# Kernel tuning notes

Hardware: AMD Instinct MI355X
Metric: run time of the kernel (lower is better)

## Reference

```python
import jax, jax.numpy as jnp
import numpy as np

B, T, E, H, W = 2, 1024, 1024, 8, 31
D = 2 * W + 1  # head dim must equal 2*window_size+1 for the rel-pos broadcast


def _ln(x, w, b):
    mu = jnp.mean(x, axis=-1, keepdims=True)
    var = jnp.mean(jnp.square(x - mu), axis=-1, keepdims=True)
    return (x - mu) * jax.lax.rsqrt(var + 1e-5) * w + b


def setup_inputs() -> dict:
    key = jax.random.key(0)
    k = jax.random.split(key, 8)
    s = 0.02
    return {
        "x": jax.random.normal(k[0], (B, T, E // 2), jnp.float32),
        "ln1_w": jnp.ones(E, jnp.float32), "ln1_b": jnp.zeros(E, jnp.float32),
        "qkv_w": jax.random.normal(k[1], (3 * H * D, E), jnp.float32) * s,
        "qkv_b": jnp.zeros(3 * H * D, jnp.float32),
        "rel_pos": jax.random.normal(k[2], (D, D), jnp.float32) * s,
        "proj_w": jax.random.normal(k[3], (E, H * D), jnp.float32) * s,
        "proj_b": jnp.zeros(E, jnp.float32),
        "ln2_w": jnp.ones(E, jnp.float32), "ln2_b": jnp.zeros(E, jnp.float32),
        "fc_w": jax.random.normal(k[4], (4 * E, E), jnp.float32) * s,
        "fc_b": jnp.zeros(4 * E, jnp.float32),
        "cproj_w": jax.random.normal(k[5], (E, 4 * E), jnp.float32) * s,
        "cproj_b": jnp.zeros(E, jnp.float32),
    }


def reference(x, ln1_w, ln1_b, qkv_w, qkv_b, rel_pos, proj_w, proj_b,
              ln2_w, ln2_b, fc_w, fc_b, cproj_w, cproj_b):
    # --- RotaryEmbedding: angle = x * inv_freq; out = cat(sin, cos) -> [B,T,E]
    dim = 2 * x.shape[-1]
    inv_freq = 1.0 / 10000.0 ** (jnp.arange(0, dim, 2, dtype=jnp.float32) / dim)
    ang = x * inv_freq
    xr = jnp.concatenate([jnp.sin(ang), jnp.cos(ang)], axis=-1)  # [B,T,E]

    # --- custom windowed attention on ln_1(xr)
    h = _ln(xr, ln1_w, ln1_b)
    qkv = h @ qkv_w.T + qkv_b                       # [B,T,3*H*D]
    q, k, v = jnp.split(qkv, 3, axis=-1)

    def heads(t):
        return t.reshape(B, T, H, D).transpose(0, 2, 1, 3)  # [B,H,T,D]

    q, k, v = heads(q), heads(k), heads(v)
    # per-token q-outer-k scores (einsum '...bd,...bv->...bdv'): [B,H,T,D,D]
    scores = jnp.einsum('bhtd,bhtv->bhtdv', q, k)
    # rel-pos bias: Embedding lookup at offsets -W..W (negative indices wrap)
    bias = rel_pos[jnp.arange(-W, W + 1) % D]       # [D, D] == [2W+1, d_model]
    attn = jax.nn.softmax(scores + bias, axis=-2)   # softmax over non-canonical axis
    out = jnp.einsum('bhtdv,bhtv->bhtd', attn, v)   # apply per-token attn matrix to v
    out = out.transpose(0, 2, 1, 3).reshape(B, T, H * D)
    xa = xr + out @ proj_w.T + proj_b               # residual

    # --- MLP
    h2 = _ln(xa, ln2_w, ln2_b)
    m = jax.nn.gelu(h2 @ fc_w.T + fc_b, approximate=False) @ cproj_w.T + cproj_b
    return xa + m
```

## Files before the change

### kernel.cpp

```cpp
#include <hip/hip_runtime.h>
#include <hip/hip_bf16.h>


typedef __bf16 bf16;
typedef bf16 bf16x8 __attribute__((ext_vector_type(8)));
typedef bf16 bf16x4 __attribute__((ext_vector_type(4)));
typedef bf16 bf16x2 __attribute__((ext_vector_type(2)));
typedef float f32x4 __attribute__((ext_vector_type(4)));

__device__ __forceinline__ float rdlane(float x, int l)
{
    return __int_as_float(__builtin_amdgcn_readlane(__float_as_int(x), l));
}

__global__ __launch_bounds__(256) void rotary_ln_kernel(
    const float* __restrict__ x, const float* __restrict__ w,
    const float* __restrict__ b, float* __restrict__ xr, bf16* __restrict__ Y)
{
    const int row = blockIdx.x;
    const int tid = threadIdx.x;
    float2 xv = *(const float2*)(x + (size_t)row * 512 + tid * 2);
    float i0 = exp2f(-(float)(2*tid)     * 0.025952563241307518f);
    float i1 = exp2f(-(float)(2*tid + 1) * 0.025952563241307518f);
    float a0 = xv.x * i0, a1 = xv.y * i1;
    float s0 = sinf(a0), s1 = sinf(a1);
    float c0 = cosf(a0), c1 = cosf(a1);
    *(float2*)(xr + (size_t)row * 1024 + tid*2)       = make_float2(s0, s1);
    *(float2*)(xr + (size_t)row * 1024 + 512 + tid*2) = make_float2(c0, c1);
    float s  = s0 + s1 + c0 + c1;
    float ss = s0*s0 + s1*s1 + c0*c0 + c1*c1;
    #pragma unroll
    for (int off = 32; off > 0; off >>= 1) {
        s  += __shfl_down(s, off);
        ss += __shfl_down(ss, off);
    }
    __shared__ float rs[4], rss[4];
    int wave = tid >> 6, lane = tid & 63;
    if (lane == 0) { rs[wave] = s; rss[wave] = ss; }
    __syncthreads();
    s  = rs[0] + rs[1] + rs[2] + rs[3];
    ss = rss[0] + rss[1] + rss[2] + rss[3];
    float mu   = s * (1.f / 1024.f);
    float var  = ss * (1.f / 1024.f) - mu * mu;
    float rstd = rsqrtf(var + 1e-5f);
    float2 w0 = *(const float2*)(w + tid*2);
    float2 b0 = *(const float2*)(b + tid*2);
    float2 w1 = *(const float2*)(w + 512 + tid*2);
    float2 b1 = *(const float2*)(b + 512 + tid*2);
    bf16x2 y0, y1;
    y0[0] = (bf16)((s0 - mu) * rstd * w0.x + b0.x);
    y0[1] = (bf16)((s1 - mu) * rstd * w0.y + b0.y);
    y1[0] = (bf16)((c0 - mu) * rstd * w1.x + b1.x);
    y1[1] = (bf16)((c1 - mu) * rstd * w1.y + b1.y);
    *(bf16x2*)(Y + (size_t)row * 1024 + tid*2)       = y0;
    *(bf16x2*)(Y + (size_t)row * 1024 + 512 + tid*2) = y1;
}

__device__ __forceinline__ void conv_chunk(
    const float* __restrict__ src, bf16* __restrict__ dst,
    int ci, int N, int K, int Kp)
{
    int kpc = Kp >> 3;
    int r  = ci / kpc;
    int kc = (ci - r * kpc) << 3;
    bf16x8 o;
    if (r < N && kc < K) {
        float4 f0 = *(const float4*)(src + (size_t)r * K + kc);
        float4 f1 = *(const float4*)(src + (size_t)r * K + kc + 4);
        o[0]=(bf16)f0.x; o[1]=(bf16)f0.y; o[2]=(bf16)f0.z; o[3]=(bf16)f0.w;
        o[4]=(bf16)f1.x; o[5]=(bf16)f1.y; o[6]=(bf16)f1.z; o[7]=(bf16)f1.w;
    } else {
        #pragma unroll
        for (int j = 0; j < 8; ++j) o[j] = (bf16)0.f;
    }
    *(bf16x8*)(dst + (size_t)r * Kp + kc) = o;
}

__global__ __launch_bounds__(256) void conv_all_kernel(
    const float* __restrict__ qkv_w, const float* __restrict__ proj_w,
    const float* __restrict__ fc_w,  const float* __restrict__ cproj_w,
    const float* __restrict__ qkv_b,
    bf16* __restrict__ wqkv, bf16* __restrict__ wproj,
    bf16* __restrict__ wfc,  bf16* __restrict__ wcproj,
    float* __restrict__ qkvb_p)
{
    if (blockIdx.x == 5120) {
        for (int i = threadIdx.x; i < 1536; i += 256)
            qkvb_p[i] = (i < 1512) ? qkv_b[i] : 0.f;
        return;
    }
    int idx = blockIdx.x * 256 + threadIdx.x;
    if      (idx < 196608)  conv_chunk(qkv_w,   wqkv,   idx,          1512, 1024, 1024);
    else if (idx < 262144)  conv_chunk(proj_w,  wproj,  idx - 196608, 1024,  504,  512);
    else if (idx < 786432)  conv_chunk(fc_w,    wfc,    idx - 262144, 4096, 1024, 1024);
    else                    conv_chunk(cproj_w, wcproj, idx - 786432, 1024, 4096, 4096);
}

template<int N> __device__ __forceinline__ void vmwait()
{
    if constexpr      (N==0) asm volatile("s_waitcnt vmcnt(0)" ::: "memory");
    else if constexpr (N==3) asm volatile("s_waitcnt vmcnt(3)" ::: "memory");
    else if constexpr (N==4) asm volatile("s_waitcnt vmcnt(4)" ::: "memory");
}
__device__ __forceinline__ void lgkmwait0()
{
    asm volatile("s_waitcnt lgkmcnt(0)" ::: "memory");
}
__device__ __forceinline__ void hw_barrier()
{
    asm volatile("s_barrier" ::: "memory");
}
__device__ __forceinline__ void gload16(const char* src, char* ldsdst)
{
    __builtin_amdgcn_global_load_lds(
        (const __attribute__((address_space(1))) void*)src,
        (__attribute__((address_space(3))) void*)ldsdst, 16, 0, 0);
}
__device__ __forceinline__ float gelu_exact(float v)
{
    return 0.5f * v * (1.f + erff(v * 0.70710678118654752f));
}

template<int EPI>
__global__ __launch_bounds__(256, 3) void gemm9_kernel(
    const bf16* __restrict__ A, const bf16* __restrict__ Wt,
    const float* __restrict__ bias, bf16* __restrict__ Cb,
    int N, int Kp, int ksplit)
{
    __shared__ __align__(16) char lds[3][16384];

    const int tid  = threadIdx.x;
    const int w    = tid >> 6;
    const int lane = tid & 63;

    const int gx = gridDim.x, gy = gridDim.y;
    const int nwg = gx * gy * gridDim.z;
    const int chunk = nwg >> 3;
    int id = (blockIdx.z * gy + blockIdx.y) * gx + blockIdx.x;
    int sw = (id & 7) * chunk + (id >> 3);
    const int bx = sw % gx;
    const int t2 = sw / gx;
    const int by = t2 % gy;
    const int bz = t2 / gy;

    const int row0 = by * 128;
    const int col0 = bx * 128;
    const int wr = (w >> 1) * 64;
    const int wc = (w & 1) * 64;
    const int rl = lane & 15;
    const int slotR = lane >> 4;

    const size_t strideBy = (size_t)Kp * 2;
    const size_t kz = (size_t)bz * ksplit * 2;
    const char* Abase = (const char*)A  + (size_t)row0 * strideBy + kz;
    const char* Wbase = (const char*)Wt + (size_t)col0 * strideBy + kz;

    size_t srcA[2];
    #pragma unroll
    for (int i = 0; i < 2; ++i) {
        int ch = i * 256 + tid;
        int r  = ch >> 2;
        int s  = (ch & 3) ^ ((r >> 1) & 3);
        srcA[i] = (size_t)r * strideBy + (size_t)(s << 4);
    }

    f32x4 acc[4][4] = {};

    auto STAGE = [&](int buf, int kt) {
        const char* ab = Abase + (size_t)kt * 64;
        const char* wb = Wbase + (size_t)kt * 64;
        #pragma unroll
        for (int i = 0; i < 2; ++i)
            gload16(ab + srcA[i], &lds[buf][0]    + (i * 256 + tid) * 16);
        #pragma unroll
        for (int i = 0; i < 2; ++i)
            gload16(wb + srcA[i], &lds[buf][8192] + (i * 256 + tid) * 16);
    };

    const int niter = ksplit >> 5;
    STAGE(0, 0);
    STAGE(1, 1);
    vmwait<4>();
    hw_barrier();

    int cur = 0, stg = 2;
    for (int kt = 0; kt < niter; ++kt) {
        if (kt + 2 < niter) STAGE(stg, kt + 2);
        const char* base = lds[cur];
        bf16x8 af[4], bfr[4];
        #pragma unroll
        for (int mi = 0; mi < 4; ++mi) {
            int r = wr + mi * 16 + rl;
            af[mi] = *(const bf16x8*)
                (base + (r << 6) + ((slotR ^ ((r >> 1) & 3)) << 4));
        }
        #pragma unroll
        for (int nj = 0; nj < 4; ++nj) {
            int r = wc + nj * 16 + rl;
            bfr[nj] = *(const bf16x8*)
                (base + 8192 + (r << 6) + ((slotR ^ ((r >> 1) & 3)) << 4));
        }
        hw_barrier();
        lgkmwait0();
        __builtin_amdgcn_s_setprio(1);
        #pragma unroll
        for (int mi = 0; mi < 4; ++mi)
            #pragma unroll
            for (int nj = 0; nj < 4; ++nj)
                acc[mi][nj] = __builtin_amdgcn_mfma_f32_16x16x32_bf16(
                    af[mi], bfr[nj], acc[mi][nj], 0, 0, 0);
        __builtin_amdgcn_s_setprio(0);

        if (kt + 1 < niter) {
            if (kt + 2 < niter) vmwait<4>();
            else                vmwait<0>();
            hw_barrier();
        }
        cur = (cur == 2) ? 0 : cur + 1;
        stg = (stg == 2) ? 0 : stg + 1;
    }

    const int rq = (lane >> 4) * 4;
    bf16* Cbz = Cb;
    if (EPI == 3) Cbz += (size_t)bz * 2048 * N;
    #pragma unroll
    for (int mi = 0; mi < 4; ++mi) {
        #pragma unroll
        for (int rj = 0; rj < 4; ++rj) {
            int row = row0 + wr + mi*16 + rq + rj;
            #pragma unroll
            for (int nj = 0; nj < 4; ++nj) {
                int col = col0 + wc + nj*16 + rl;
                float c = acc[mi][nj][rj];
                size_t off = (size_t)row * N + col;
                if (EPI == 0)      Cbz[off] = (bf16)(c + bias[col]);
                else if (EPI == 1) Cbz[off] = (bf16)gelu_exact(c + bias[col]);
                else               Cbz[off] = (bf16)c;
            }
        }
    }
}

template<int EPI>
__global__ __launch_bounds__(256, 4) void gemm7_kernel(
    const bf16* __restrict__ A, const bf16* __restrict__ Wt,
    const float* __restrict__ bias, bf16* __restrict__ Cb,
    int N, int Kp, int ksplit)
{
    __shared__ __align__(16) char lds[3][12288];

    const int tid  = threadIdx.x;
    const int w    = tid >> 6;
    const int lane = tid & 63;

    const int gx = gridDim.x, gy = gridDim.y;
    const int nwg = gx * gy * gridDim.z;
    const int chunk = nwg >> 3;
    int id = (blockIdx.z * gy + blockIdx.y) * gx + blockIdx.x;
    int sw = (id & 7) * chunk + (id >> 3);
    const int bx = sw % gx;
    const int t2 = sw / gx;
    const int by = t2 % gy;
    const int bz = t2 / gy;

    const int row0 = by * 64;
    const int col0 = bx * 128;
    const int wr = (w >> 1) * 32;
    const int wc = (w & 1) * 64;
    const int rl = lane & 15;
    const int slotR = lane >> 4;

    const size_t strideBy = (size_t)Kp * 2;
    const size_t kz = (size_t)bz * ksplit * 2;
    const char* Abase = (const char*)A  + (size_t)row0 * strideBy + kz;
    const char* Wbase = (const char*)Wt + (size_t)col0 * strideBy + kz;

    const int arow = tid >> 2;
    const size_t srcA0 = (size_t)arow * strideBy
                       + (size_t)(((tid & 3) ^ ((arow >> 1) & 3)) << 4);
    size_t srcB[2];
    #pragma unroll
    for (int i = 0; i < 2; ++i) {
        int o = (i * 256 + tid) * 16;
        int r = o >> 6;
        int s = ((o & 63) >> 4) ^ ((r >> 1) & 3);
        srcB[i] = (size_t)r * strideBy + (size_t)(s << 4);
    }

    f32x4 acc[2][4] = {};

    auto STAGE = [&](int buf, int kt) {
        const char* ab = Abase + (size_t)kt * 64;
        const char* wb = Wbase + (size_t)kt * 64;
        gload16(ab + srcA0, &lds[buf][0] + tid * 16);
        #pragma unroll
        for (int i = 0; i < 2; ++i)
            gload16(wb + srcB[i], &lds[buf][4096] + (i * 256 + tid) * 16);
    };

    const int niter = ksplit >> 5;
    STAGE(0, 0);
    STAGE(1, 1);
    vmwait<3>();
    hw_barrier();

    int cur = 0, stg = 2;
    for (int kt = 0; kt < niter; ++kt) {
        if (kt + 2 < niter) STAGE(stg, kt + 2);
        const char* base = lds[cur];
        bf16x8 af[2], bfr[4];
        #pragma unroll
        for (int mi = 0; mi < 2; ++mi) {
            int r = wr + mi * 16 + rl;
            af[mi] = *(const bf16x8*)
                (base + (r << 6) + ((slotR ^ ((r >> 1) & 3)) << 4));
        }
        #pragma unroll
        for (int nj = 0; nj < 4; ++nj) {
            int r = wc + nj * 16 + rl;
            bfr[nj] = *(const bf16x8*)
                (base + 4096 + (r << 6) + ((slotR ^ ((r >> 1) & 3)) << 4));
        }
        __builtin_amdgcn_s_setprio(1);
        #pragma unroll
        for (int mi = 0; mi < 2; ++mi)
            #pragma unroll
            for (int nj = 0; nj < 4; ++nj)
                acc[mi][nj] = __builtin_amdgcn_mfma_f32_16x16x32_bf16(
                    af[mi], bfr[nj], acc[mi][nj], 0, 0, 0);
        __builtin_amdgcn_s_setprio(0);

        if (kt + 1 < niter) {
            lgkmwait0();
            if (kt + 2 < niter) vmwait<3>();
            else                vmwait<0>();
            hw_barrier();
        }
        cur = (cur == 2) ? 0 : cur + 1;
        stg = (stg == 2) ? 0 : stg + 1;
    }

    const int rq = (lane >> 4) * 4;
    bf16* Cbz = Cb;
    if (EPI == 3) Cbz += (size_t)bz * 2048 * N;
    #pragma unroll
    for (int mi = 0; mi < 2; ++mi) {
        #pragma unroll
        for (int rj = 0; rj < 4; ++rj) {
            int row = row0 + wr + mi*16 + rq + rj;
            #pragma unroll
            for (int nj = 0; nj < 4; ++nj) {
                int col = col0 + wc + nj*16 + rl;
                float c = acc[mi][nj][rj];
                size_t off = (size_t)row * N + col;
                if (EPI == 0)      Cbz[off] = (bf16)(c + bias[col]);
                else if (EPI == 1) Cbz[off] = (bf16)gelu_exact(c + bias[col]);
                else               Cbz[off] = (bf16)c;
            }
        }
    }
}

template<int P>
__global__ __launch_bounds__(256) void reduce_kernel(
    const bf16* __restrict__ parts, const float* __restrict__ bias,
    const float* R, float* out)
{
    int row = blockIdx.x;
    int c = threadIdx.x * 4;
    size_t off = (size_t)row * 1024 + c;
    float4 bv = *(const float4*)(bias + c);
    float4 o = *(const float4*)(R + off);
    o.x += bv.x; o.y += bv.y; o.z += bv.z; o.w += bv.w;
    #pragma unroll
    for (int p = 0; p < P; ++p) {
        bf16x4 v = *(const bf16x4*)(parts + (size_t)p * 2048 * 1024 + off);
        o.x += (float)v[0]; o.y += (float)v[1];
        o.z += (float)v[2]; o.w += (float)v[3];
    }
    *(float4*)(out + off) = o;
}

__global__ __launch_bounds__(256) void reduceln_kernel(
    const bf16* __restrict__ parts, const float* __restrict__ bias,
    const float* __restrict__ R, const float* __restrict__ lnw,
    const float* __restrict__ lnb, float* __restrict__ out,
    bf16* __restrict__ Y)
{
    int row = blockIdx.x;
    int c = threadIdx.x * 4;
    size_t off = (size_t)row * 1024 + c;
    float4 bv = *(const float4*)(bias + c);
    float4 o  = *(const float4*)(R + off);
    o.x += bv.x; o.y += bv.y; o.z += bv.z; o.w += bv.w;
    #pragma unroll
    for (int p = 0; p < 2; ++p) {
        bf16x4 v = *(const bf16x4*)(parts + (size_t)p * 2048 * 1024 + off);
        o.x += (float)v[0]; o.y += (float)v[1];
        o.z += (float)v[2]; o.w += (float)v[3];
    }
    *(float4*)(out + off) = o;
    float s  = o.x + o.y + o.z + o.w;
    float ss = o.x*o.x + o.y*o.y + o.z*o.z + o.w*o.w;
    #pragma unroll
    for (int of = 32; of > 0; of >>= 1) {
        s  += __shfl_down(s, of);
        ss += __shfl_down(ss, of);
    }
    __shared__ float rs[4], rss[4];
    int wave = threadIdx.x >> 6, lane = threadIdx.x & 63;
    if (lane == 0) { rs[wave] = s; rss[wave] = ss; }
    __syncthreads();
    s  = rs[0] + rs[1] + rs[2] + rs[3];
    ss = rss[0] + rss[1] + rss[2] + rss[3];
    float mu  = s * (1.f / 1024.f);
    float var = ss * (1.f / 1024.f) - mu * mu;
    float rstd = rsqrtf(var + 1e-5f);
    float4 wv = *(const float4*)(lnw + c);
    float4 lb = *(const float4*)(lnb + c);
    bf16 y[4];
    y[0] = (bf16)((o.x - mu) * rstd * wv.x + lb.x);
    y[1] = (bf16)((o.y - mu) * rstd * wv.y + lb.y);
    y[2] = (bf16)((o.z - mu) * rstd * wv.z + lb.z);
    y[3] = (bf16)((o.w - mu) * rstd * wv.w + lb.w);
    *(uint2*)(Y + (size_t)row * 1024 + c) = *(uint2*)y;
}

__global__ __launch_bounds__(1024) void attn3_kernel(
    const bf16* __restrict__ qkv, const float* __restrict__ rel_pos,
    bf16* __restrict__ outp)
{
    __shared__ float bR[4096];
    __shared__ float bT[4096];
    for (int i = threadIdx.x; i < 4096; i += 1024) {
        int d = i >> 6, v = i & 63;
        float val = (d < 63 && v < 63)
                  ? rel_pos[((d + 32) % 63) * 63 + v] * 1.4426950408889634f
                  : -1e30f;
        bR[(d << 6) + (((v >> 2) ^ (d & 15)) << 2) + (v & 3)] = val;
        bT[(v << 6) + (((d >> 2) ^ (v & 15)) << 2) + (d & 3)] = val;
    }
    __syncthreads();

    const int wave = threadIdx.x >> 6;
    const int lane = threadIdx.x & 63;
    const int tk  = blockIdx.x * 16 + wave;
    const int row = tk >> 3;
    const int h   = tk & 7;
    const bf16* base = qkv + (size_t)row * 1536 + h * 63;
    float q_own = 0.f, k_own = 0.f, v_own = 0.f;
    if (lane < 63) {
        q_own = (float)base[lane] * 1.4426950408889634f;
        k_own = (float)base[504 + lane];
        v_own = (float)base[1008 + lane];
    }

    const float* myT = bT + (lane << 6);
    const int sw = lane & 15;
    float z0 = 0.f, z1 = 0.f, z2 = 0.f, z3 = 0.f;
    #pragma unroll
    for (int g = 0; g < 16; ++g) {
        f32x4 bb = *(const f32x4*)(myT + ((g ^ sw) << 2));
        z0 += __builtin_amdgcn_exp2f(fmaf(rdlane(q_own, 4*g + 0), k_own, bb[0]));
        z1 += __builtin_amdgcn_exp2f(fmaf(rdlane(q_own, 4*g + 1), k_own, bb[1]));
        z2 += __builtin_amdgcn_exp2f(fmaf(rdlane(q_own, 4*g + 2), k_own, bb[2]));
        z3 += __builtin_amdgcn_exp2f(fmaf(rdlane(q_own, 4*g + 3), k_own, bb[3]));
    }
    float Z = (z0 + z1) + (z2 + z3);
    float w_own = (lane < 63) ? v_own / Z : 0.f;

    const float* myR = bR + (lane << 6);
    float a0 = 0.f, a1 = 0.f, a2 = 0.f, a3 = 0.f;
    #pragma unroll
    for (int g = 0; g < 16; ++g) {
        f32x4 bb = *(const f32x4*)(myR + ((g ^ sw) << 2));
        a0 = fmaf(__builtin_amdgcn_exp2f(fmaf(q_own, rdlane(k_own, 4*g + 0), bb[0])),
                  rdlane(w_own, 4*g + 0), a0);
        a1 = fmaf(__builtin_amdgcn_exp2f(fmaf(q_own, rdlane(k_own, 4*g + 1), bb[1])),
                  rdlane(w_own, 4*g + 1), a1);
        a2 = fmaf(__builtin_amdgcn_exp2f(fmaf(q_own, rdlane(k_own, 4*g + 2), bb[2])),
                  rdlane(w_own, 4*g + 2), a2);
        a3 = fmaf(__builtin_amdgcn_exp2f(fmaf(q_own, rdlane(k_own, 4*g + 3), bb[3])),
                  rdlane(w_own, 4*g + 3), a3);
    }
    float acc = (a0 + a1) + (a2 + a3);

    if (lane < 63)
        outp[(size_t)row * 512 + h*63 + lane] = (bf16)acc;
    if (h == 7 && lane == 63) {
        #pragma unroll
        for (int j = 0; j < 8; ++j)
            outp[(size_t)row * 512 + 504 + j] = (bf16)0.f;
    }
}

extern "C" void kernel_launch(void* const* d_in, const int* in_sizes, int n_in,
                              void* d_out, int out_size, void* d_ws, size_t ws_size,
                              hipStream_t stream)
{
    const float* x       = (const float*)d_in[0];
    const float* ln1_w   = (const float*)d_in[1];
    const float* ln1_b   = (const float*)d_in[2];
    const float* qkv_w   = (const float*)d_in[3];
    const float* qkv_b   = (const float*)d_in[4];
    const float* rel_pos = (const float*)d_in[5];
    const float* proj_w  = (const float*)d_in[6];
    const float* proj_b  = (const float*)d_in[7];
    const float* ln2_w   = (const float*)d_in[8];
    const float* ln2_b   = (const float*)d_in[9];
    const float* fc_w    = (const float*)d_in[10];
    const float* fc_b    = (const float*)d_in[11];
    const float* cproj_w = (const float*)d_in[12];
    const float* cproj_b = (const float*)d_in[13];
    float* out = (float*)d_out;

    char* p = (char*)d_ws;
    float* xr      = (float*)p;            p += (size_t)2048*1024*4;
    bf16*  h_bf    = (bf16*)p;             p += (size_t)2048*1024*2;
    bf16*  wqkv    = (bf16*)p;             p += (size_t)1536*1024*2;
    bf16*  wproj   = (bf16*)p;             p += (size_t)1024*512*2;
    bf16*  wfc     = (bf16*)p;             p += (size_t)4096*1024*2;
    bf16*  wcproj  = (bf16*)p;             p += (size_t)1024*4096*2;
    float* qkvb_p  = (float*)p;            p += 8192;
    bf16*  attn_bf = (bf16*)p;             p += (size_t)2048*512*2;
    bf16*  qkvb    = (bf16*)p;
    bf16*  fc_act  = (bf16*)p;
    bf16*  proj_part = qkvb;
    bf16*  cp_part = (bf16*)d_ws;

    conv_all_kernel<<<5121, 256, 0, stream>>>(qkv_w, proj_w, fc_w, cproj_w, qkv_b,
                                              wqkv, wproj, wfc, wcproj, qkvb_p);
    rotary_ln_kernel<<<2048, 256, 0, stream>>>(x, ln1_w, ln1_b, xr, h_bf);
    gemm7_kernel<0><<<dim3(12,32,1), 256, 0, stream>>>(h_bf, wqkv, qkvb_p,
                                                       qkvb, 1536, 1024, 1024);
    attn3_kernel<<<1024, 1024, 0, stream>>>(qkvb, rel_pos, attn_bf);
    gemm7_kernel<3><<<dim3(8,32,2), 256, 0, stream>>>(attn_bf, wproj, nullptr,
                                                      proj_part, 1024, 512, 256);
    reduceln_kernel<<<2048, 256, 0, stream>>>(proj_part, proj_b, xr,
                                              ln2_w, ln2_b, out, h_bf);
    gemm9_kernel<1><<<dim3(32,16,1), 256, 0, stream>>>(h_bf, wfc, fc_b,
                                                       fc_act, 4096, 1024, 1024);
    gemm9_kernel<3><<<dim3(8,16,4), 256, 0, stream>>>(fc_act, wcproj, nullptr,
                                                      cp_part, 1024, 4096, 1024);
    reduce_kernel<4><<<2048, 256, 0, stream>>>(cp_part, cproj_b, out, out);
}
```

Baseline: 136.9 us.

## Use 512-thread 8-wave blocks for MLP GEMMs and drop mid-loop barrier

```diff
diff --git a/kernel.cpp b/kernel.cpp
--- a/kernel.cpp
+++ b/kernel.cpp
@@ -99,6 +99,7 @@
 template<int N> __device__ __forceinline__ void vmwait()
 {
     if constexpr      (N==0) asm volatile("s_waitcnt vmcnt(0)" ::: "memory");
+    else if constexpr (N==2) asm volatile("s_waitcnt vmcnt(2)" ::: "memory");
     else if constexpr (N==3) asm volatile("s_waitcnt vmcnt(3)" ::: "memory");
     else if constexpr (N==4) asm volatile("s_waitcnt vmcnt(4)" ::: "memory");
 }
@@ -122,7 +123,7 @@
 }
 
 template<int EPI>
-__global__ __launch_bounds__(256, 3) void gemm9_kernel(
+__global__ __launch_bounds__(512, 4) void gemm11_kernel(
     const bf16* __restrict__ A, const bf16* __restrict__ Wt,
     const float* __restrict__ bias, bf16* __restrict__ Cb,
     int N, int Kp, int ksplit)
@@ -132,6 +133,10 @@
     const int tid  = threadIdx.x;
     const int w    = tid >> 6;
     const int lane = tid & 63;
+    const int wm   = w >> 2;
+    const int wn   = w & 3;
+    const int rl   = lane & 15;
+    const int slotR = lane >> 4;
 
     const int gx = gridDim.x, gy = gridDim.y;
     const int nwg = gx * gy * gridDim.z;
@@ -145,79 +150,61 @@
 
     const int row0 = by * 128;
     const int col0 = bx * 128;
-    const int wr = (w >> 1) * 64;
-    const int wc = (w & 1) * 64;
-    const int rl = lane & 15;
-    const int slotR = lane >> 4;
-
     const size_t strideBy = (size_t)Kp * 2;
     const size_t kz = (size_t)bz * ksplit * 2;
     const char* Abase = (const char*)A  + (size_t)row0 * strideBy + kz;
     const char* Wbase = (const char*)Wt + (size_t)col0 * strideBy + kz;
 
-    size_t srcA[2];
-    #pragma unroll
-    for (int i = 0; i < 2; ++i) {
-        int ch = i * 256 + tid;
-        int r  = ch >> 2;
-        int s  = (ch & 3) ^ ((r >> 1) & 3);
-        srcA[i] = (size_t)r * strideBy + (size_t)(s << 4);
-    }
-
-    f32x4 acc[4][4] = {};
+    const int r  = tid >> 2;
+    const int s  = (tid & 3) ^ ((r >> 1) & 3);
+    const size_t srcOff = (size_t)r * strideBy + (size_t)(s << 4);
+
+    f32x4 acc[4][2] = {};
 
     auto STAGE = [&](int buf, int kt) {
         const char* ab = Abase + (size_t)kt * 64;
         const char* wb = Wbase + (size_t)kt * 64;
-        #pragma unroll
-        for (int i = 0; i < 2; ++i)
-            gload16(ab + srcA[i], &lds[buf][0]    + (i * 256 + tid) * 16);
-        #pragma unroll
-        for (int i = 0; i < 2; ++i)
-            gload16(wb + srcA[i], &lds[buf][8192] + (i * 256 + tid) * 16);
+        gload16(ab + srcOff, &lds[buf][0]    + tid * 16);
+        gload16(wb + srcOff, &lds[buf][8192] + tid * 16);
     };
 
     const int niter = ksplit >> 5;
     STAGE(0, 0);
     STAGE(1, 1);
-    vmwait<4>();
+    vmwait<2>();
     hw_barrier();
 
-    int cur = 0, stg = 2;
     for (int kt = 0; kt < niter; ++kt) {
-        if (kt + 2 < niter) STAGE(stg, kt + 2);
-        const char* base = lds[cur];
-        bf16x8 af[4], bfr[4];
+        if (kt + 2 < niter) STAGE((kt + 2) % 3, kt + 2);
+        const char* base = lds[kt % 3];
+        bf16x8 af[4], bfr[2];
         #pragma unroll
         for (int mi = 0; mi < 4; ++mi) {
-            int r = wr + mi * 16 + rl;
+            int rr = wm * 64 + mi * 16 + rl;
             af[mi] = *(const bf16x8*)
-                (base + (r << 6) + ((slotR ^ ((r >> 1) & 3)) << 4));
-        }
-        #pragma unroll
-        for (int nj = 0; nj < 4; ++nj) {
-            int r = wc + nj * 16 + rl;
+                (base + (rr << 6) + ((slotR ^ ((rr >> 1) & 3)) << 4));
+        }
+        #pragma unroll
+        for (int nj = 0; nj < 2; ++nj) {
+            int rr = wn * 32 + nj * 16 + rl;
             bfr[nj] = *(const bf16x8*)
-                (base + 8192 + (r << 6) + ((slotR ^ ((r >> 1) & 3)) << 4));
-        }
-        hw_barrier();
+                (base + 8192 + (rr << 6) + ((slotR ^ ((rr >> 1) & 3)) << 4));
+        }
         lgkmwait0();
         __builtin_amdgcn_s_setprio(1);
         #pragma unroll
         for (int mi = 0; mi < 4; ++mi)
             #pragma unroll
-            for (int nj = 0; nj < 4; ++nj)
+            for (int nj = 0; nj < 2; ++nj)
                 acc[mi][nj] = __builtin_amdgcn_mfma_f32_16x16x32_bf16(
                     af[mi], bfr[nj], acc[mi][nj], 0, 0, 0);
         __builtin_amdgcn_s_setprio(0);
 
         if (kt + 1 < niter) {
-            if (kt + 2 < niter) vmwait<4>();
+            if (kt + 2 < niter) vmwait<2>();
             else                vmwait<0>();
             hw_barrier();
         }
-        cur = (cur == 2) ? 0 : cur + 1;
-        stg = (stg == 2) ? 0 : stg + 1;
     }
 
     const int rq = (lane >> 4) * 4;
@@ -227,15 +214,14 @@
     for (int mi = 0; mi < 4; ++mi) {
         #pragma unroll
         for (int rj = 0; rj < 4; ++rj) {
-            int row = row0 + wr + mi*16 + rq + rj;
+            int row = row0 + wm * 64 + mi * 16 + rq + rj;
             #pragma unroll
-            for (int nj = 0; nj < 4; ++nj) {
-                int col = col0 + wc + nj*16 + rl;
+            for (int nj = 0; nj < 2; ++nj) {
+                int col = col0 + wn * 32 + nj * 16 + rl;
                 float c = acc[mi][nj][rj];
                 size_t off = (size_t)row * N + col;
-                if (EPI == 0)      Cbz[off] = (bf16)(c + bias[col]);
-                else if (EPI == 1) Cbz[off] = (bf16)gelu_exact(c + bias[col]);
-                else               Cbz[off] = (bf16)c;
+                if (EPI == 1) Cbz[off] = (bf16)gelu_exact(c + bias[col]);
+                else          Cbz[off] = (bf16)c;
             }
         }
     }
@@ -282,9 +268,9 @@
     #pragma unroll
     for (int i = 0; i < 2; ++i) {
         int o = (i * 256 + tid) * 16;
-        int r = o >> 6;
-        int s = ((o & 63) >> 4) ^ ((r >> 1) & 3);
-        srcB[i] = (size_t)r * strideBy + (size_t)(s << 4);
+        int rr = o >> 6;
+        int ss = ((o & 63) >> 4) ^ ((rr >> 1) & 3);
+        srcB[i] = (size_t)rr * strideBy + (size_t)(ss << 4);
     }
 
     f32x4 acc[2][4] = {};
@@ -311,15 +297,15 @@
         bf16x8 af[2], bfr[4];
         #pragma unroll
         for (int mi = 0; mi < 2; ++mi) {
-            int r = wr + mi * 16 + rl;
+            int rr = wr + mi * 16 + rl;
             af[mi] = *(const bf16x8*)
-                (base + (r << 6) + ((slotR ^ ((r >> 1) & 3)) << 4));
+                (base + (rr << 6) + ((slotR ^ ((rr >> 1) & 3)) << 4));
         }
         #pragma unroll
         for (int nj = 0; nj < 4; ++nj) {
-            int r = wc + nj * 16 + rl;
+            int rr = wc + nj * 16 + rl;
             bfr[nj] = *(const bf16x8*)
-                (base + 4096 + (r << 6) + ((slotR ^ ((r >> 1) & 3)) << 4));
+                (base + 4096 + (rr << 6) + ((slotR ^ ((rr >> 1) & 3)) << 4));
         }
         __builtin_amdgcn_s_setprio(1);
         #pragma unroll
@@ -538,9 +524,9 @@
                                                       proj_part, 1024, 512, 256);
     reduceln_kernel<<<2048, 256, 0, stream>>>(proj_part, proj_b, xr,
                                               ln2_w, ln2_b, out, h_bf);
-    gemm9_kernel<1><<<dim3(32,16,1), 256, 0, stream>>>(h_bf, wfc, fc_b,
-                                                       fc_act, 4096, 1024, 1024);
-    gemm9_kernel<3><<<dim3(8,16,4), 256, 0, stream>>>(fc_act, wcproj, nullptr,
-                                                      cp_part, 1024, 4096, 1024);
+    gemm11_kernel<1><<<dim3(32,16,1), 512, 0, stream>>>(h_bf, wfc, fc_b,
+                                                        fc_act, 4096, 1024, 1024);
+    gemm11_kernel<3><<<dim3(8,16,4), 512, 0, stream>>>(fc_act, wcproj, nullptr,
+                                                       cp_part, 1024, 4096, 1024);
     reduce_kernel<4><<<2048, 256, 0, stream>>>(cp_part, cproj_b, out, out);
 }
```

Result: faster. 133.7 us (-2.3%).
